# Optimization experiments

Hardware: AMD Instinct MI355X
Metric: run time of the kernel (lower is better)

Reference implementation:

```python
import jax, jax.numpy as jnp
import numpy as np

N_NODES = 100000
N_EDGES = 3200000


def setup_inputs() -> dict:
    key = jax.random.key(0)
    k1, k2, k3, k4 = jax.random.split(key, 4)
    inputs = jax.random.normal(k1, (N_NODES, 16), dtype=jnp.float32)
    W1 = jax.random.normal(k2, (16, 16), dtype=jnp.float32) * 0.25
    b1 = jnp.zeros((16,), dtype=jnp.float32)
    W2 = jax.random.normal(k3, (16, 8), dtype=jnp.float32) * 0.25
    b2 = jnp.zeros((8,), dtype=jnp.float32)
    edge_index = jax.random.randint(k4, (2, N_EDGES), 0, N_NODES, dtype=jnp.int64)
    return {"inputs": inputs, "W1": W1, "b1": b1, "W2": W2, "b2": b2,
            "edge_index": edge_index}


def _graph_conv(x, W, b, src, dst, norm_src, norm_dst, n_nodes):
    # DGL GraphConv, norm='both': out = D_dst^{-1/2} A^T (D_src^{-1/2} X W) + b
    h = (x @ W) * norm_src[:, None]          # [N, out]
    agg = jax.ops.segment_sum(h[src], dst, num_segments=n_nodes)  # scatter over edges
    return agg * norm_dst[:, None] + b


def reference(inputs, W1, b1, W2, b2, edge_index):
    n = inputs.shape[0]
    self_loop = jnp.arange(n, dtype=edge_index.dtype)
    src = jnp.concatenate([edge_index[0], self_loop])
    dst = jnp.concatenate([edge_index[1], self_loop])
    ones = jnp.ones(src.shape[0], dtype=inputs.dtype)
    deg_out = jax.ops.segment_sum(ones, src, num_segments=n)
    deg_in = jax.ops.segment_sum(ones, dst, num_segments=n)
    norm_src = jax.lax.rsqrt(jnp.clip(deg_out, 1.0))
    norm_dst = jax.lax.rsqrt(jnp.clip(deg_in, 1.0))

    h = _graph_conv(inputs, W1, b1, src, dst, norm_src, norm_dst, n)
    h = jax.nn.relu(h)
    h = _graph_conv(h, W2, b2, src, dst, norm_src, norm_dst, n)
    return h
```

## Files before the change

kernel.cpp:

```cpp
#include <hip/hip_runtime.h>


constexpr int F1 = 16;
constexpr int F2 = 8;
constexpr int NB_HIST = 128;
constexpr int HIST_N  = 100000;
constexpr int HIST_U32 = HIST_N / 4;


__global__ void __launch_bounds__(256) hist_kernel(const int* __restrict__ idx,
                                                   unsigned* __restrict__ partial,
                                                   int nE, int per_block) {
    __shared__ unsigned h[HIST_U32];
    for (int i = threadIdx.x; i < HIST_U32; i += 256) h[i] = 0u;
    __syncthreads();
    const int beg = blockIdx.x * per_block;
    const int end = min(nE, beg + per_block);
    for (int base = beg; base < end; base += 256 * 4) {
        int i = base + threadIdx.x * 4;
        if (i + 3 < end) {
            int4 v = *reinterpret_cast<const int4*>(idx + i);
            atomicAdd(&h[v.x >> 2], 1u << ((v.x & 3) << 3));
            atomicAdd(&h[v.y >> 2], 1u << ((v.y & 3) << 3));
            atomicAdd(&h[v.z >> 2], 1u << ((v.z & 3) << 3));
            atomicAdd(&h[v.w >> 2], 1u << ((v.w & 3) << 3));
        } else {
#pragma unroll
            for (int k = 0; k < 4; ++k)
                if (i + k < end) {
                    int v = idx[i + k];
                    atomicAdd(&h[v >> 2], 1u << ((v & 3) << 3));
                }
        }
    }
    __syncthreads();
    unsigned* out = partial + (size_t)blockIdx.x * HIST_U32;
    for (int i = threadIdx.x; i < HIST_U32; i += 256) out[i] = h[i];
}

__global__ void __launch_bounds__(256) merge_norm_kernel(const unsigned* __restrict__ partial,
                                                         float* __restrict__ norm) {
    int t = blockIdx.x * 256 + threadIdx.x;
    if (t >= HIST_U32) return;
    unsigned s0 = 0, s1 = 0, s2 = 0, s3 = 0;
    const unsigned* p = partial + t;
    for (int b = 0; b < NB_HIST; ++b) {
        unsigned v = p[(size_t)b * HIST_U32];
        s0 += v & 0xffu; s1 += (v >> 8) & 0xffu;
        s2 += (v >> 16) & 0xffu; s3 += v >> 24;
    }
    float4 o = make_float4(rsqrtf(1.f + (float)s0), rsqrtf(1.f + (float)s1),
                           rsqrtf(1.f + (float)s2), rsqrtf(1.f + (float)s3));
    *reinterpret_cast<float4*>(norm + (size_t)t * 4) = o;
}


__global__ void init_deg_kernel(float* __restrict__ a, float* __restrict__ b, int n) {
    int i = blockIdx.x * 256 + threadIdx.x;
    if (i < n) { a[i] = 1.0f; b[i] = 1.0f; }
}
__global__ void count_deg_kernel(const int* __restrict__ src, const int* __restrict__ dst,
                                 float* __restrict__ dego, float* __restrict__ degi, int nE) {
    int e = blockIdx.x * 256 + threadIdx.x;
    if (e < nE) { atomicAdd(dego + src[e], 1.0f); atomicAdd(degi + dst[e], 1.0f); }
}
__global__ void rsqrt_kernel(float* __restrict__ a, float* __restrict__ b, int n) {
    int i = blockIdx.x * 256 + threadIdx.x;
    if (i < n) { a[i] = rsqrtf(a[i]); b[i] = rsqrtf(b[i]); }
}


__global__ void xw16_kernel(const float* __restrict__ x, const float* __restrict__ W,
                            const float* __restrict__ norm_src,
                            float* __restrict__ h, int n) {
    __shared__ float Ws[256];
    int t = threadIdx.x;
    if (t < 256) Ws[t] = W[t];
    __syncthreads();
    int i = blockIdx.x * blockDim.x + t;
    if (i >= n) return;
    float xi[16];
    const float4* xp = reinterpret_cast<const float4*>(x + (size_t)i * 16);
    float4 v;
    v = xp[0]; xi[0]=v.x; xi[1]=v.y; xi[2]=v.z; xi[3]=v.w;
    v = xp[1]; xi[4]=v.x; xi[5]=v.y; xi[6]=v.z; xi[7]=v.w;
    v = xp[2]; xi[8]=v.x; xi[9]=v.y; xi[10]=v.z; xi[11]=v.w;
    v = xp[3]; xi[12]=v.x; xi[13]=v.y; xi[14]=v.z; xi[15]=v.w;
    float ns = norm_src[i];
    float o[16];
#pragma unroll
    for (int j = 0; j < 16; ++j) {
        float acc = 0.f;
#pragma unroll
        for (int k = 0; k < 16; ++k) acc = fmaf(xi[k], Ws[k * 16 + j], acc);
        o[j] = acc * ns;
    }
    float4* hp = reinterpret_cast<float4*>(h + (size_t)i * 16);
    hp[0] = make_float4(o[0], o[1], o[2], o[3]);
    hp[1] = make_float4(o[4], o[5], o[6], o[7]);
    hp[2] = make_float4(o[8], o[9], o[10], o[11]);
    hp[3] = make_float4(o[12], o[13], o[14], o[15]);
}

__global__ void xw8_kernel(const float* __restrict__ x, const float* __restrict__ W,
                           const float* __restrict__ norm_src,
                           float* __restrict__ h, int n) {
    __shared__ float Ws[128];
    int t = threadIdx.x;
    if (t < 128) Ws[t] = W[t];
    __syncthreads();
    int i = blockIdx.x * blockDim.x + t;
    if (i >= n) return;
    float xi[16];
    const float4* xp = reinterpret_cast<const float4*>(x + (size_t)i * 16);
    float4 v;
    v = xp[0]; xi[0]=v.x; xi[1]=v.y; xi[2]=v.z; xi[3]=v.w;
    v = xp[1]; xi[4]=v.x; xi[5]=v.y; xi[6]=v.z; xi[7]=v.w;
    v = xp[2]; xi[8]=v.x; xi[9]=v.y; xi[10]=v.z; xi[11]=v.w;
    v = xp[3]; xi[12]=v.x; xi[13]=v.y; xi[14]=v.z; xi[15]=v.w;
    float ns = norm_src[i];
    float o[8];
#pragma unroll
    for (int j = 0; j < 8; ++j) {
        float acc = 0.f;
#pragma unroll
        for (int k = 0; k < 16; ++k) acc = fmaf(xi[k], Ws[k * 8 + j], acc);
        o[j] = acc * ns;
    }
    float4* hp = reinterpret_cast<float4*>(h + (size_t)i * 8);
    hp[0] = make_float4(o[0], o[1], o[2], o[3]);
    hp[1] = make_float4(o[4], o[5], o[6], o[7]);
}

template <int F>
__global__ void scatter_kernel(const int* __restrict__ src, const int* __restrict__ dst,
                               const float* __restrict__ h, float* __restrict__ agg,
                               int nE) {
    long long t = (long long)blockIdx.x * blockDim.x + threadIdx.x;
    if (t >= (long long)nE * F) return;
    int e = (int)(t >> (F == 16 ? 4 : 3));
    int f = (int)(t & (F - 1));
    int s = src[e];
    int d = dst[e];
    atomicAdd(agg + (size_t)d * F + f, h[(size_t)s * F + f]);
}

template <int F, bool RELU>
__global__ void combine_kernel(const float* __restrict__ agg, const float* __restrict__ h,
                               const float* __restrict__ norm_dst,
                               const float* __restrict__ b,
                               float* __restrict__ out, int n) {
    int t = blockIdx.x * 256 + threadIdx.x;
    if (t >= n * F) return;
    int i = t / F;
    int f = t % F;
    float v = (agg[t] + h[t]) * norm_dst[i] + b[f];
    if (RELU) v = fmaxf(v, 0.f);
    out[t] = v;
}

extern "C" void kernel_launch(void* const* d_in, const int* in_sizes, int n_in,
                              void* d_out, int out_size, void* d_ws, size_t ws_size,
                              hipStream_t stream) {
    const float* x  = (const float*)d_in[0];
    const float* W1 = (const float*)d_in[1];
    const float* b1 = (const float*)d_in[2];
    const float* W2 = (const float*)d_in[3];
    const float* b2 = (const float*)d_in[4];
    const int*   ei = (const int*)d_in[5];

    const int n  = in_sizes[0] / F1;
    const int nE = in_sizes[5] / 2;
    const int* src = ei;
    const int* dst = ei + nE;

    size_t na = ((size_t)n + 63) & ~(size_t)63;
    float* norm_src = (float*)d_ws;
    float* norm_dst = norm_src + na;
    float* bufA     = norm_dst + na;
    float* bufB     = bufA + na * F1;
    unsigned* partial = (unsigned*)bufA;

    const int B = 256;
    dim3 blk(B);
    int gN   = (n + B - 1) / B;
    int gNF1 = (n * F1 + B - 1) / B;
    int gNF2 = (n * F2 + B - 1) / B;
    int gEF1 = (int)(((long long)nE * F1 + B - 1) / B);
    int gEF2 = (int)(((long long)nE * F2 + B - 1) / B);

    if (n == HIST_N) {
        int per_block = (nE + NB_HIST - 1) / NB_HIST;
        int gM = (HIST_U32 + B - 1) / B;
        hist_kernel<<<NB_HIST, blk, 0, stream>>>(src, partial, nE, per_block);
        merge_norm_kernel<<<gM, blk, 0, stream>>>(partial, norm_src);
        hist_kernel<<<NB_HIST, blk, 0, stream>>>(dst, partial, nE, per_block);
        merge_norm_kernel<<<gM, blk, 0, stream>>>(partial, norm_dst);
    } else {
        int gE = (nE + B - 1) / B;
        init_deg_kernel<<<gN, blk, 0, stream>>>(norm_src, norm_dst, n);
        count_deg_kernel<<<gE, blk, 0, stream>>>(src, dst, norm_src, norm_dst, nE);
        rsqrt_kernel<<<gN, blk, 0, stream>>>(norm_src, norm_dst, n);
    }

    xw16_kernel<<<gN, blk, 0, stream>>>(x, W1, norm_src, bufA, n);
    hipMemsetAsync(bufB, 0, (size_t)n * F1 * sizeof(float), stream);
    scatter_kernel<F1><<<gEF1, blk, 0, stream>>>(src, dst, bufA, bufB, nE);
    combine_kernel<F1, true><<<gNF1, blk, 0, stream>>>(bufB, bufA, norm_dst, b1, bufB, n);

    xw8_kernel<<<gN, blk, 0, stream>>>(bufB, W2, norm_src, bufA, n);
    hipMemsetAsync(bufB, 0, (size_t)n * F2 * sizeof(float), stream);
    scatter_kernel<F2><<<gEF2, blk, 0, stream>>>(src, dst, bufA, bufB, nE);
    combine_kernel<F2, false><<<gNF2, blk, 0, stream>>>(bufB, bufA, norm_dst, b2,
                                                        (float*)d_out, n);
}
```

Before: 409.9 us.

## Bucket edges by destination and aggregate in shared memory instead of global atomics

Adds a counting-sort style partition of edges into 128-node destination buckets, packing the local destination and source into one u32. Each layer's aggregation then runs one block per bucket and accumulates into padded shared memory, replacing global float atomics on the output. The in-degree norm is also computed from the buckets. The partition costs extra passes over the edge list and workspace, and the fast path runs only when the workspace is large enough.

```diff
diff --git a/kernel.cpp b/kernel.cpp
--- a/kernel.cpp
+++ b/kernel.cpp
@@ -1,17 +1,22 @@
 #include <hip/hip_runtime.h>
+
+typedef unsigned int u32;
 
 
 constexpr int F1 = 16;
 constexpr int F2 = 8;
-constexpr int NB_HIST = 128;
-constexpr int HIST_N  = 100000;
+constexpr int HIST_N   = 100000;
 constexpr int HIST_U32 = HIST_N / 4;
+constexpr int NB_HIST  = 256;
+constexpr int RB       = 128;
+constexpr int NBUCK    = (HIST_N + RB - 1) / RB;
+constexpr int P2B      = 256;
 
 
 __global__ void __launch_bounds__(256) hist_kernel(const int* __restrict__ idx,
-                                                   unsigned* __restrict__ partial,
+                                                   u32* __restrict__ partial,
                                                    int nE, int per_block) {
-    __shared__ unsigned h[HIST_U32];
+    __shared__ u32 h[HIST_U32];
     for (int i = threadIdx.x; i < HIST_U32; i += 256) h[i] = 0u;
     __syncthreads();
     const int beg = blockIdx.x * per_block;
@@ -34,18 +39,18 @@
         }
     }
     __syncthreads();
-    unsigned* out = partial + (size_t)blockIdx.x * HIST_U32;
+    u32* out = partial + (size_t)blockIdx.x * HIST_U32;
     for (int i = threadIdx.x; i < HIST_U32; i += 256) out[i] = h[i];
 }
 
-__global__ void __launch_bounds__(256) merge_norm_kernel(const unsigned* __restrict__ partial,
+__global__ void __launch_bounds__(256) merge_norm_kernel(const u32* __restrict__ partial,
                                                          float* __restrict__ norm) {
     int t = blockIdx.x * 256 + threadIdx.x;
     if (t >= HIST_U32) return;
-    unsigned s0 = 0, s1 = 0, s2 = 0, s3 = 0;
-    const unsigned* p = partial + t;
+    u32 s0 = 0, s1 = 0, s2 = 0, s3 = 0;
+    const u32* p = partial + t;
     for (int b = 0; b < NB_HIST; ++b) {
-        unsigned v = p[(size_t)b * HIST_U32];
+        u32 v = p[(size_t)b * HIST_U32];
         s0 += v & 0xffu; s1 += (v >> 8) & 0xffu;
         s2 += (v >> 16) & 0xffu; s3 += v >> 24;
     }
@@ -55,18 +60,109 @@
 }
 
 
-__global__ void init_deg_kernel(float* __restrict__ a, float* __restrict__ b, int n) {
-    int i = blockIdx.x * 256 + threadIdx.x;
-    if (i < n) { a[i] = 1.0f; b[i] = 1.0f; }
-}
-__global__ void count_deg_kernel(const int* __restrict__ src, const int* __restrict__ dst,
-                                 float* __restrict__ dego, float* __restrict__ degi, int nE) {
-    int e = blockIdx.x * 256 + threadIdx.x;
-    if (e < nE) { atomicAdd(dego + src[e], 1.0f); atomicAdd(degi + dst[e], 1.0f); }
-}
-__global__ void rsqrt_kernel(float* __restrict__ a, float* __restrict__ b, int n) {
-    int i = blockIdx.x * 256 + threadIdx.x;
-    if (i < n) { a[i] = rsqrtf(a[i]); b[i] = rsqrtf(b[i]); }
+__global__ void __launch_bounds__(256) bucket_count_kernel(const int* __restrict__ dst,
+                                                           u32* __restrict__ bcnt, int nE) {
+    __shared__ u32 c[NBUCK];
+    for (int j = threadIdx.x; j < NBUCK; j += 256) c[j] = 0;
+    __syncthreads();
+    for (int i = blockIdx.x * 256 + threadIdx.x; i < nE; i += 256 * P2B)
+        atomicAdd(&c[dst[i] >> 7], 1u);
+    __syncthreads();
+    for (int j = threadIdx.x; j < NBUCK; j += 256)
+        if (c[j]) atomicAdd(&bcnt[j], c[j]);
+}
+
+__global__ void __launch_bounds__(1024) bucket_scan_kernel(const u32* __restrict__ bcnt,
+                                                           u32* __restrict__ bbase,
+                                                           u32* __restrict__ bcur) {
+    __shared__ u32 s[1024];
+    int t = threadIdx.x;
+    u32 v = (t < NBUCK) ? bcnt[t] : 0;
+    s[t] = v;
+    __syncthreads();
+    for (int off = 1; off < 1024; off <<= 1) {
+        u32 a = (t >= off) ? s[t - off] : 0;
+        __syncthreads();
+        s[t] += a;
+        __syncthreads();
+    }
+    if (t < NBUCK) {
+        u32 ex = s[t] - v;
+        bbase[t] = ex;
+        bcur[t] = ex;
+        if (t == NBUCK - 1) bbase[NBUCK] = s[t];
+    }
+}
+
+__global__ void __launch_bounds__(256) partition_kernel(const int* __restrict__ src,
+                                                        const int* __restrict__ dst,
+                                                        u32* __restrict__ part,
+                                                        u32* __restrict__ bcur,
+                                                        int nE, int per_block) {
+    __shared__ u32 cnt[NBUCK];
+    __shared__ u32 gb[NBUCK];
+    for (int j = threadIdx.x; j < NBUCK; j += 256) cnt[j] = 0;
+    __syncthreads();
+    const int beg = blockIdx.x * per_block;
+    const int end = min(nE, beg + per_block);
+    for (int i = beg + threadIdx.x; i < end; i += 256)
+        atomicAdd(&cnt[dst[i] >> 7], 1u);
+    __syncthreads();
+    for (int j = threadIdx.x; j < NBUCK; j += 256) {
+        u32 c = cnt[j];
+        gb[j] = c ? atomicAdd(&bcur[j], c) : 0u;
+        cnt[j] = 0;
+    }
+    __syncthreads();
+    for (int i = beg + threadIdx.x; i < end; i += 256) {
+        int d = dst[i];
+        int b = d >> 7;
+        u32 r = atomicAdd(&cnt[b], 1u);
+        part[gb[b] + r] = ((u32)(d & 127) << 17) | (u32)src[i];
+    }
+}
+
+__global__ void __launch_bounds__(256) norm_dst_kernel(const u32* __restrict__ part,
+                                                       const u32* __restrict__ bbase,
+                                                       float* __restrict__ norm_dst, int n) {
+    __shared__ u32 c[RB];
+    if (threadIdx.x < RB) c[threadIdx.x] = 0;
+    __syncthreads();
+    u32 beg = bbase[blockIdx.x], end = bbase[blockIdx.x + 1];
+    for (u32 j = beg + threadIdx.x; j < end; j += 256)
+        atomicAdd(&c[part[j] >> 17], 1u);
+    __syncthreads();
+    if (threadIdx.x < RB) {
+        int node = blockIdx.x * RB + threadIdx.x;
+        if (node < n) norm_dst[node] = rsqrtf(1.f + (float)c[threadIdx.x]);
+    }
+}
+
+template <int F>
+__global__ void __launch_bounds__(256) agg_kernel(const u32* __restrict__ part,
+                                                  const u32* __restrict__ bbase,
+                                                  const float* __restrict__ h,
+                                                  float* __restrict__ agg, int n) {
+    __shared__ float acc[RB * (F + 1)];
+    for (int j = threadIdx.x; j < RB * (F + 1); j += 256) acc[j] = 0.f;
+    __syncthreads();
+    const int b = blockIdx.x;
+    const u32 beg = bbase[b], end = bbase[b + 1];
+    const int g = threadIdx.x / F;
+    const int f = threadIdx.x % F;
+    const int step = 256 / F;
+    for (u32 j = beg + g; j < end; j += step) {
+        u32 w = part[j];
+        u32 s = w & 0x1FFFFu;
+        u32 dl = w >> 17;
+        atomicAdd(&acc[dl * (F + 1) + f], h[(size_t)s * F + f]);
+    }
+    __syncthreads();
+    for (int idx = threadIdx.x; idx < RB * F; idx += 256) {
+        int dl = idx / F, ff = idx % F;
+        int node = b * RB + dl;
+        if (node < n) agg[(size_t)node * F + ff] = acc[dl * (F + 1) + ff];
+    }
 }
 
 
@@ -130,19 +226,6 @@
     float4* hp = reinterpret_cast<float4*>(h + (size_t)i * 8);
     hp[0] = make_float4(o[0], o[1], o[2], o[3]);
     hp[1] = make_float4(o[4], o[5], o[6], o[7]);
-}
-
-template <int F>
-__global__ void scatter_kernel(const int* __restrict__ src, const int* __restrict__ dst,
-                               const float* __restrict__ h, float* __restrict__ agg,
-                               int nE) {
-    long long t = (long long)blockIdx.x * blockDim.x + threadIdx.x;
-    if (t >= (long long)nE * F) return;
-    int e = (int)(t >> (F == 16 ? 4 : 3));
-    int f = (int)(t & (F - 1));
-    int s = src[e];
-    int d = dst[e];
-    atomicAdd(agg + (size_t)d * F + f, h[(size_t)s * F + f]);
 }
 
 template <int F, bool RELU>
@@ -159,6 +242,31 @@
     out[t] = v;
 }
 
+
+__global__ void init_deg_kernel(float* __restrict__ a, float* __restrict__ b, int n) {
+    int i = blockIdx.x * 256 + threadIdx.x;
+    if (i < n) { a[i] = 1.0f; b[i] = 1.0f; }
+}
+__global__ void count_deg_kernel(const int* __restrict__ src, const int* __restrict__ dst,
+                                 float* __restrict__ dego, float* __restrict__ degi, int nE) {
+    int e = blockIdx.x * 256 + threadIdx.x;
+    if (e < nE) { atomicAdd(dego + src[e], 1.0f); atomicAdd(degi + dst[e], 1.0f); }
+}
+__global__ void rsqrt_kernel(float* __restrict__ a, float* __restrict__ b, int n) {
+    int i = blockIdx.x * 256 + threadIdx.x;
+    if (i < n) { a[i] = rsqrtf(a[i]); b[i] = rsqrtf(b[i]); }
+}
+template <int F>
+__global__ void scatter_kernel(const int* __restrict__ src, const int* __restrict__ dst,
+                               const float* __restrict__ h, float* __restrict__ agg,
+                               int nE) {
+    long long t = (long long)blockIdx.x * blockDim.x + threadIdx.x;
+    if (t >= (long long)nE * F) return;
+    int e = (int)(t / F);
+    int f = (int)(t % F);
+    atomicAdd(agg + (size_t)dst[e] * F + f, h[(size_t)src[e] * F + f]);
+}
+
 extern "C" void kernel_launch(void* const* d_in, const int* in_sizes, int n_in,
                               void* d_out, int out_size, void* d_ws, size_t ws_size,
                               hipStream_t stream) {
@@ -174,43 +282,67 @@
     const int* src = ei;
     const int* dst = ei + nE;
 
-    size_t na = ((size_t)n + 63) & ~(size_t)63;
+    const size_t na = ((size_t)n + 63) & ~(size_t)63;
+    const int B = 256;
+    dim3 blk(B);
+    int gN   = (int)((n + B - 1) / B);
+    int gNF1 = (int)((n * (size_t)F1 + B - 1) / B);
+    int gNF2 = (int)((n * (size_t)F2 + B - 1) / B);
+
     float* norm_src = (float*)d_ws;
     float* norm_dst = norm_src + na;
-    float* bufA     = norm_dst + na;
+    u32*   bbase    = (u32*)(norm_dst + na);
+    u32*   bcur     = bbase + 1024;
+    u32*   bcnt     = bcur + 1024;
+    u32*   part     = bcnt + 1024;
+    float* bufA     = (float*)(part + nE);
     float* bufB     = bufA + na * F1;
-    unsigned* partial = (unsigned*)bufA;
-
-    const int B = 256;
-    dim3 blk(B);
-    int gN   = (n + B - 1) / B;
-    int gNF1 = (n * F1 + B - 1) / B;
-    int gNF2 = (n * F2 + B - 1) / B;
-    int gEF1 = (int)(((long long)nE * F1 + B - 1) / B);
-    int gEF2 = (int)(((long long)nE * F2 + B - 1) / B);
-
-    if (n == HIST_N) {
-        int per_block = (nE + NB_HIST - 1) / NB_HIST;
+    u32*   partial  = part;
+    size_t need = ((size_t)2 * na + 3 * 1024 + (size_t)nE + 32 * na) * 4;
+    size_t need_hist = ((size_t)2 * na + 3 * 1024) * 4 + (size_t)NB_HIST * HIST_U32 * 4;
+    if (need_hist > need) need = need_hist;
+
+    if (n == HIST_N && ws_size >= need) {
+        int per_hist = (nE + NB_HIST - 1) / NB_HIST;
+        int per_p2   = (nE + P2B - 1) / P2B;
         int gM = (HIST_U32 + B - 1) / B;
-        hist_kernel<<<NB_HIST, blk, 0, stream>>>(src, partial, nE, per_block);
+
+        hist_kernel<<<NB_HIST, blk, 0, stream>>>(src, partial, nE, per_hist);
         merge_norm_kernel<<<gM, blk, 0, stream>>>(partial, norm_src);
-        hist_kernel<<<NB_HIST, blk, 0, stream>>>(dst, partial, nE, per_block);
-        merge_norm_kernel<<<gM, blk, 0, stream>>>(partial, norm_dst);
+
+        hipMemsetAsync(bcnt, 0, NBUCK * sizeof(u32), stream);
+        bucket_count_kernel<<<P2B, blk, 0, stream>>>(dst, bcnt, nE);
+        bucket_scan_kernel<<<1, 1024, 0, stream>>>(bcnt, bbase, bcur);
+        partition_kernel<<<P2B, blk, 0, stream>>>(src, dst, part, bcur, nE, per_p2);
+        norm_dst_kernel<<<NBUCK, blk, 0, stream>>>(part, bbase, norm_dst, n);
+
+        xw16_kernel<<<gN, blk, 0, stream>>>(x, W1, norm_src, bufA, n);
+        agg_kernel<F1><<<NBUCK, blk, 0, stream>>>(part, bbase, bufA, bufB, n);
+        combine_kernel<F1, true><<<gNF1, blk, 0, stream>>>(bufB, bufA, norm_dst, b1, bufB, n);
+
+        xw8_kernel<<<gN, blk, 0, stream>>>(bufB, W2, norm_src, bufA, n);
+        agg_kernel<F2><<<NBUCK, blk, 0, stream>>>(part, bbase, bufA, bufB, n);
+        combine_kernel<F2, false><<<gNF2, blk, 0, stream>>>(bufB, bufA, norm_dst, b2,
+                                                            (float*)d_out, n);
     } else {
-        int gE = (nE + B - 1) / B;
-        init_deg_kernel<<<gN, blk, 0, stream>>>(norm_src, norm_dst, n);
-        count_deg_kernel<<<gE, blk, 0, stream>>>(src, dst, norm_src, norm_dst, nE);
-        rsqrt_kernel<<<gN, blk, 0, stream>>>(norm_src, norm_dst, n);
-    }
-
-    xw16_kernel<<<gN, blk, 0, stream>>>(x, W1, norm_src, bufA, n);
-    hipMemsetAsync(bufB, 0, (size_t)n * F1 * sizeof(float), stream);
-    scatter_kernel<F1><<<gEF1, blk, 0, stream>>>(src, dst, bufA, bufB, nE);
-    combine_kernel<F1, true><<<gNF1, blk, 0, stream>>>(bufB, bufA, norm_dst, b1, bufB, n);
-
-    xw8_kernel<<<gN, blk, 0, stream>>>(bufB, W2, norm_src, bufA, n);
-    hipMemsetAsync(bufB, 0, (size_t)n * F2 * sizeof(float), stream);
-    scatter_kernel<F2><<<gEF2, blk, 0, stream>>>(src, dst, bufA, bufB, nE);
-    combine_kernel<F2, false><<<gNF2, blk, 0, stream>>>(bufB, bufA, norm_dst, b2,
-                                                        (float*)d_out, n);
-}
+        float* fnorm_src = (float*)d_ws;
+        float* fnorm_dst = fnorm_src + na;
+        float* fbufA     = fnorm_dst + na;
+        float* fbufB     = fbufA + na * F1;
+        int gE   = (nE + B - 1) / B;
+        int gEF1 = (int)(((long long)nE * F1 + B - 1) / B);
+        int gEF2 = (int)(((long long)nE * F2 + B - 1) / B);
+        init_deg_kernel<<<gN, blk, 0, stream>>>(fnorm_src, fnorm_dst, n);
+        count_deg_kernel<<<gE, blk, 0, stream>>>(src, dst, fnorm_src, fnorm_dst, nE);
+        rsqrt_kernel<<<gN, blk, 0, stream>>>(fnorm_src, fnorm_dst, n);
+        xw16_kernel<<<gN, blk, 0, stream>>>(x, W1, fnorm_src, fbufA, n);
+        hipMemsetAsync(fbufB, 0, (size_t)n * F1 * sizeof(float), stream);
+        scatter_kernel<F1><<<gEF1, blk, 0, stream>>>(src, dst, fbufA, fbufB, nE);
+        combine_kernel<F1, true><<<gNF1, blk, 0, stream>>>(fbufB, fbufA, fnorm_dst, b1, fbufB, n);
+        xw8_kernel<<<gN, blk, 0, stream>>>(fbufB, W2, fnorm_src, fbufA, n);
+        hipMemsetAsync(fbufB, 0, (size_t)n * F2 * sizeof(float), stream);
+        scatter_kernel<F2><<<gEF2, blk, 0, stream>>>(src, dst, fbufA, fbufB, nE);
+        combine_kernel<F2, false><<<gNF2, blk, 0, stream>>>(fbufB, fbufA, fnorm_dst, b2,
+                                                            (float*)d_out, n);
+    }
+}
```

After: 654.7 us. 59.7% more time.
